# Kernel tuning notes

Measured on AMD Instinct MI355X. Metric: run time of the kernel, lower is better.

## Reference

```python
import jax, jax.numpy as jnp
import numpy as np

B, T, D, H = 2, 2048, 1024, 16
DK = D // H


def setup_inputs() -> dict:
    key = jax.random.key(0)
    ks = jax.random.split(key, 11)
    s = 1.0 / np.sqrt(D)
    return {
        "x_q": jax.random.normal(ks[0], (B, T, D), jnp.float32),
        "x_kv": jax.random.normal(ks[1], (B, T, D), jnp.float32),
        "mask": jnp.ones((B, 1, T, T), jnp.int32),
        "Wq": jax.random.normal(ks[2], (D, D), jnp.float32) * s,
        "bq": jnp.zeros((D,), jnp.float32),
        "Wk": jax.random.normal(ks[3], (D, D), jnp.float32) * s,
        "bk": jnp.zeros((D,), jnp.float32),
        "Wv": jax.random.normal(ks[4], (D, D), jnp.float32) * s,
        "bv": jnp.zeros((D,), jnp.float32),
        "Wo": jax.random.normal(ks[5], (D, D), jnp.float32) * s,
        "bo": jnp.zeros((D,), jnp.float32),
    }


def _split_heads(x):
    # (B, T, D) -> (B, H, T, DK)
    b, t, _ = x.shape
    return x.reshape(b, t, H, DK).transpose(0, 2, 1, 3)


def reference(x_q, x_kv, mask, Wq, bq, Wk, bk, Wv, bv, Wo, bo):
    # Linear layers use torch convention: y = x @ W.T + b
    Q = _split_heads(x_q @ Wq.T + bq)   # (B,H,Tq,DK)
    K = _split_heads(x_kv @ Wk.T + bk)  # (B,H,Tk,DK)
    V = _split_heads(x_kv @ Wv.T + bv)  # (B,H,Tk,DK)

    scores = jnp.einsum("bhqd,bhkd->bhqk", Q, K) / jnp.sqrt(jnp.float32(DK))
    scores = jnp.where(mask == 0, jnp.float32(-jnp.inf), scores)
    attn = jax.nn.softmax(scores, axis=-1)  # (B,H,Tq,Tk)

    out = jnp.einsum("bhqk,bhkd->bhqd", attn, V)
    out = out.transpose(0, 2, 1, 3).reshape(B, T, D)  # combine heads
    out = out @ Wo.T + bo
    return out, attn
```

## Files before the change

kernel.cpp:

```cpp
#include <hip/hip_runtime.h>
#include <hip/hip_bf16.h>

#define DEVINL __device__ __forceinline__

typedef __attribute__((ext_vector_type(4))) float f32x4;
typedef __attribute__((ext_vector_type(8))) short short8;
typedef __attribute__((ext_vector_type(4))) short short4v;

constexpr int CB = 2, CT = 2048, CD = 1024, CH = 16, CDK = 64;
constexpr int CM = CB * CT;
constexpr float LOG2E = 1.44269504088896340736f;

DEVINL ushort f2bf(float f) {
  __hip_bfloat16 h = __float2bfloat16(f);
  ushort u; __builtin_memcpy(&u, &h, 2); return u;
}

DEVINL float bf2f(ushort u) {
  uint x = ((uint)u) << 16; float f; __builtin_memcpy(&f, &x, 4); return f;
}

DEVINL void gl2lds16(const ushort* g, ushort* ldsbase) {
  __builtin_amdgcn_global_load_lds(
      (const __attribute__((address_space(1))) void*)g,
      (__attribute__((address_space(3))) void*)ldsbase, 16, 0, 0);
}

__global__ void prep_kernel(const float* __restrict__ s0, ushort* __restrict__ d0, int n0,
                            const float* __restrict__ s1, ushort* __restrict__ d1, int n1,
                            const float* __restrict__ s2, ushort* __restrict__ d2, int n2,
                            const float* __restrict__ s3, ushort* __restrict__ d3, int n3,
                            const float* __restrict__ s4, ushort* __restrict__ d4, int n4,
                            const float* __restrict__ s5, ushort* __restrict__ d5, int n5,
                            const int* __restrict__ mask, uint* __restrict__ flags,
                            int cvt_blocks)
{
  if ((int)blockIdx.x >= cvt_blocks) {
    const int tile = blockIdx.x - cvt_blocks;
    const int b = tile >> 10, qb = (tile >> 5) & 31, kb = tile & 31;
    const int* base = mask + ((size_t)b * CT + qb * 64) * CT + kb * 64;
    const int r = threadIdx.x >> 2, c0 = (threadIdx.x & 3) * 16;
    int ok = 1;
    for (int j = 0; j < 4; ++j) {
      int4 v = *reinterpret_cast<const int4*>(base + (size_t)r * CT + c0 + j * 4);
      ok &= (v.x != 0) & (v.y != 0) & (v.z != 0) & (v.w != 0);
    }
    __shared__ int red[4];
    unsigned long long bal = __ballot(ok);
    if ((threadIdx.x & 63) == 0) red[threadIdx.x >> 6] = (bal == ~0ull);
    __syncthreads();
    if (threadIdx.x == 0) flags[tile] = (uint)(red[0] & red[1] & red[2] & red[3]);
    return;
  }
  int i = (blockIdx.x * blockDim.x + threadIdx.x) * 4;
  const float* s; ushort* d;
  if (i < n0) { s = s0; d = d0; }
  else if ((i -= n0) < n1) { s = s1; d = d1; }
  else if ((i -= n1) < n2) { s = s2; d = d2; }
  else if ((i -= n2) < n3) { s = s3; d = d3; }
  else if ((i -= n3) < n4) { s = s4; d = d4; }
  else if ((i -= n4) < n5) { s = s5; d = d5; }
  else return;
  float4 v = *reinterpret_cast<const float4*>(s + i);
  ushort4 o;
  o.x = f2bf(v.x); o.y = f2bf(v.y); o.z = f2bf(v.z); o.w = f2bf(v.w);
  *reinterpret_cast<ushort4*>(d + i) = o;
}

__global__ __launch_bounds__(256, 2)
void gemm_nt_kernel(const ushort* __restrict__ A, const ushort* __restrict__ Bm,
                    const float* __restrict__ bias1, const float* __restrict__ bias2,
                    void* __restrict__ Out, void* __restrict__ Out2,
                    int M, int N, int K, int mode, float scale)
{
  constexpr int BM = 128, BN = 64, BK = 32;
  __shared__ __align__(16) ushort As[2][BM * BK];
  __shared__ __align__(16) ushort Bs[2][BN * BK];
  const int tid = threadIdx.x;
  const int lane = tid & 63, wid = tid >> 6;
  const int wr = wid >> 1, wc = wid & 1;
  const int bm0 = blockIdx.y * BM, bn0 = blockIdx.x * BN;
  const int rsel = lane & 15, ksel = (lane >> 4) * 8;
  const int srow = lane >> 2, sc8 = (lane & 3) * 8;

  f32x4 acc[4][2];
  for (int i = 0; i < 4; ++i) for (int j = 0; j < 2; ++j) acc[i][j] = f32x4{0.f, 0.f, 0.f, 0.f};

  auto stage = [&](int bu, int k0) {
    const int ra0 = wid * 32;
    gl2lds16(&A[(size_t)(bm0 + ra0 + srow) * K + k0 + sc8],      &As[bu][ra0 * BK]);
    gl2lds16(&A[(size_t)(bm0 + ra0 + 16 + srow) * K + k0 + sc8], &As[bu][(ra0 + 16) * BK]);
    const int rb0 = wid * 16;
    gl2lds16(&Bm[(size_t)(bn0 + rb0 + srow) * K + k0 + sc8],     &Bs[bu][rb0 * BK]);
  };

  stage(0, 0);
  __syncthreads();
  const int NKT = K / BK;
  int bu = 0;
  for (int kt = 0; kt < NKT; ++kt) {
    if (kt + 1 < NKT) stage(bu ^ 1, (kt + 1) * BK);
    short8 af[4], bfr[2];
    for (int mi = 0; mi < 4; ++mi)
      af[mi] = *reinterpret_cast<short8*>(&As[bu][(wr * 64 + mi * 16 + rsel) * BK + ksel]);
    for (int ni = 0; ni < 2; ++ni)
      bfr[ni] = *reinterpret_cast<short8*>(&Bs[bu][(wc * 32 + ni * 16 + rsel) * BK + ksel]);
    for (int mi = 0; mi < 4; ++mi)
      for (int ni = 0; ni < 2; ++ni)
        acc[mi][ni] = __builtin_amdgcn_mfma_f32_16x16x32_bf16(af[mi], bfr[ni], acc[mi][ni], 0, 0, 0);
    if (kt + 1 < NKT) { __syncthreads(); bu ^= 1; }
  }

  const int r0 = (lane >> 4) * 4;
  for (int mi = 0; mi < 4; ++mi)
    for (int ni = 0; ni < 2; ++ni) {
      int gj = bn0 + wc * 32 + ni * 16 + rsel;
      float bv = (mode == 3 && gj >= 1024) ? bias2[gj - 1024] : bias1[gj];
      for (int r = 0; r < 4; ++r) {
        int gi = bm0 + wr * 64 + mi * 16 + r0 + r;
        float v = (acc[mi][ni][r] + bv) * scale;
        if (mode == 2) {
          reinterpret_cast<float*>(Out)[(size_t)gi * N + gj] = v;
        } else {
          int bb = gi >> 11, t = gi & (CT - 1);
          if (mode == 3 && gj >= 1024) {
            int gjv = gj - 1024;
            reinterpret_cast<ushort*>(Out2)[(((size_t)(bb * CH + (gjv >> 6)) * CDK + (gjv & 63)) * CT + t)] = f2bf(v);
          } else {
            reinterpret_cast<ushort*>(Out)[(((size_t)(bb * CH + (gj >> 6)) * CT + t) * CDK + (gj & 63))] = f2bf(v);
          }
        }
      }
    }
}

__global__ __launch_bounds__(512, 2)
void attn_kernel(const ushort* __restrict__ Qb, const ushort* __restrict__ Kb,
                 const ushort* __restrict__ Vt, const int* __restrict__ mask,
                 const uint* __restrict__ flags,
                 float* __restrict__ attn_out, ushort* __restrict__ oh)
{
  __shared__ __align__(16) ushort Ks[2][64 * 64];
  __shared__ __align__(16) ushort Vs[2][64 * 64];
  __shared__ __align__(16) ushort Pf[8][16 * 64];

  const int tid = threadIdx.x, wid = tid >> 6, lane = tid & 63;
  const int bh = blockIdx.y, b = bh >> 4, h = bh & 15;
  const int q0A = blockIdx.x * 256 + wid * 16;
  const int q0B = q0A + 128;
  const int rsel = lane & 15, grp = lane >> 4, ksel = grp * 8;
  const int swz = rsel & 7;
  const uint* flA = flags + (b << 10) + ((q0A >> 6) << 5);
  const uint* flB = flags + (b << 10) + ((q0B >> 6) << 5);
  const ushort* kpan = Kb + (size_t)bh * CT * CDK;
  const ushort* vpan = Vt + (size_t)bh * CDK * CT;

  const int strow = tid >> 3, stc = (tid & 7) ^ (strow & 7);

  auto stageK = [&](int bu, int k0) {
    gl2lds16(&kpan[(size_t)(k0 + strow) * CDK + stc * 8], &Ks[bu][(size_t)wid * 512]);
  };
  auto stageV = [&](int bu, int k0) {
    gl2lds16(&vpan[(size_t)strow * CT + k0 + stc * 8], &Vs[bu][(size_t)wid * 512]);
  };

  short8 qaA0, qaA1, qaB0, qaB1;
  {
    const ushort* qrowA = Qb + ((size_t)bh * CT + q0A + rsel) * CDK;
    qaA0 = *reinterpret_cast<const short8*>(qrowA + ksel);
    qaA1 = *reinterpret_cast<const short8*>(qrowA + 32 + ksel);
    const ushort* qrowB = Qb + ((size_t)bh * CT + q0B + rsel) * CDK;
    qaB0 = *reinterpret_cast<const short8*>(qrowB + ksel);
    qaB1 = *reinterpret_cast<const short8*>(qrowB + 32 + ksel);
  }

  const int* mrow = mask + (size_t)b * CT * CT;
  const int qmeA = q0A + rsel, qmeB = q0B + rsel;
  float* apan = attn_out + (size_t)bh * CT * CT;
  ushort* pw = &Pf[wid][0];

  float lA = 0.f;
  stageK(0, 0);
  __syncthreads();
  int bu = 0;
  for (int kt = 0; kt < 32; ++kt) {
    const int k0 = kt * 64;
    if (kt + 1 < 32) stageK(bu ^ 1, k0 + 64);
    const uint f = flA[kt];
    for (int ni = 0; ni < 4; ++ni) {
      const int krow = ni * 16 + rsel;
      short8 kb0 = *reinterpret_cast<short8*>(&Ks[bu][krow * 64 + ((grp    ) ^ swz) * 8]);
      short8 kb1 = *reinterpret_cast<short8*>(&Ks[bu][krow * 64 + ((grp + 4) ^ swz) * 8]);
      f32x4 z = {0.f, 0.f, 0.f, 0.f};
      z = __builtin_amdgcn_mfma_f32_16x16x32_bf16(kb0, qaA0, z, 0, 0, 0);
      z = __builtin_amdgcn_mfma_f32_16x16x32_bf16(kb1, qaA1, z, 0, 0, 0);
      if (f) {
        lA += exp2f(z[0]) + exp2f(z[1]) + exp2f(z[2]) + exp2f(z[3]);
      } else {
        const int kb_ = k0 + ni * 16 + grp * 4;
        for (int r = 0; r < 4; ++r)
          lA += mrow[(size_t)qmeA * CT + kb_ + r] ? exp2f(z[r]) : 0.f;
      }
    }
    __syncthreads();
    bu ^= 1;
  }
  lA += __shfl_xor(lA, 16, 64);
  lA += __shfl_xor(lA, 32, 64);
  const float llA = __log2f(lA);

  f32x4 oacc[4];
  for (int nd = 0; nd < 4; ++nd) oacc[nd] = f32x4{0.f, 0.f, 0.f, 0.f};
  float lB = 0.f;

  stageK(0, 0);
  stageV(0, 0);
  asm volatile("s_waitcnt vmcnt(0)" ::: "memory");
  __builtin_amdgcn_s_barrier();
  asm volatile("" ::: "memory");
  bu = 0;
  for (int kt = 0; kt < 32; ++kt) {
    const int k0 = kt * 64;
    if (kt + 1 < 32) { stageK(bu ^ 1, k0 + 64); stageV(bu ^ 1, k0 + 64); }
    asm volatile("" ::: "memory");
    const uint fA = flA[kt], fB = flB[kt];
    for (int ni = 0; ni < 4; ++ni) {
      const int krow = ni * 16 + rsel;
      short8 kb0 = *reinterpret_cast<short8*>(&Ks[bu][krow * 64 + ((grp    ) ^ swz) * 8]);
      short8 kb1 = *reinterpret_cast<short8*>(&Ks[bu][krow * 64 + ((grp + 4) ^ swz) * 8]);
      {
        f32x4 z = {0.f, 0.f, 0.f, 0.f};
        z = __builtin_amdgcn_mfma_f32_16x16x32_bf16(kb0, qaB0, z, 0, 0, 0);
        z = __builtin_amdgcn_mfma_f32_16x16x32_bf16(kb1, qaB1, z, 0, 0, 0);
        if (fB) {
          lB += exp2f(z[0]) + exp2f(z[1]) + exp2f(z[2]) + exp2f(z[3]);
        } else {
          const int kb_ = k0 + ni * 16 + grp * 4;
          for (int r = 0; r < 4; ++r)
            lB += mrow[(size_t)qmeB * CT + kb_ + r] ? exp2f(z[r]) : 0.f;
        }
      }
      f32x4 z = {0.f, 0.f, 0.f, 0.f};
      z = __builtin_amdgcn_mfma_f32_16x16x32_bf16(kb0, qaA0, z, 0, 0, 0);
      z = __builtin_amdgcn_mfma_f32_16x16x32_bf16(kb1, qaA1, z, 0, 0, 0);
      float p0, p1, p2, p3;
      if (fA) {
        p0 = exp2f(z[0] - llA); p1 = exp2f(z[1] - llA);
        p2 = exp2f(z[2] - llA); p3 = exp2f(z[3] - llA);
      } else {
        const size_t mb = (size_t)qmeA * CT + k0 + ni * 16 + grp * 4;
        p0 = mrow[mb + 0] ? exp2f(z[0] - llA) : 0.f;
        p1 = mrow[mb + 1] ? exp2f(z[1] - llA) : 0.f;
        p2 = mrow[mb + 2] ? exp2f(z[2] - llA) : 0.f;
        p3 = mrow[mb + 3] ? exp2f(z[3] - llA) : 0.f;
      }
      const int chpos = (2 * ni + (grp >> 1)) ^ swz;
      short4v pk = {(short)f2bf(p0), (short)f2bf(p1), (short)f2bf(p2), (short)f2bf(p3)};
      *reinterpret_cast<short4v*>(&pw[rsel * 64 + chpos * 8 + (grp & 1) * 4]) = pk;
    }
    for (int rr = 0; rr < 4; ++rr) {
      const int row = rr * 4 + grp;
      const int rs = row & 7;
      short4v pv4 = *reinterpret_cast<short4v*>(
          &pw[row * 64 + (((rsel >> 1) ^ rs)) * 8 + (rsel & 1) * 4]);
      f32x4 v = {bf2f((ushort)pv4[0]), bf2f((ushort)pv4[1]),
                 bf2f((ushort)pv4[2]), bf2f((ushort)pv4[3])};
      __builtin_nontemporal_store(v,
          reinterpret_cast<f32x4*>(apan + (size_t)(q0A + row) * CT + k0 + rsel * 4));
    }
    short8 pa0 = *reinterpret_cast<short8*>(&pw[rsel * 64 + ((grp    ) ^ swz) * 8]);
    short8 pa1 = *reinterpret_cast<short8*>(&pw[rsel * 64 + ((grp + 4) ^ swz) * 8]);
    for (int nd = 0; nd < 4; ++nd) {
      const int vrow = nd * 16 + rsel;
      short8 vb0 = *reinterpret_cast<short8*>(&Vs[bu][vrow * 64 + ((grp    ) ^ swz) * 8]);
      short8 vb1 = *reinterpret_cast<short8*>(&Vs[bu][vrow * 64 + ((grp + 4) ^ swz) * 8]);
      oacc[nd] = __builtin_amdgcn_mfma_f32_16x16x32_bf16(pa0, vb0, oacc[nd], 0, 0, 0);
      oacc[nd] = __builtin_amdgcn_mfma_f32_16x16x32_bf16(pa1, vb1, oacc[nd], 0, 0, 0);
    }
    asm volatile("s_waitcnt vmcnt(4)" ::: "memory");
    __builtin_amdgcn_s_barrier();
    asm volatile("" ::: "memory");
    bu ^= 1;
  }
  for (int nd = 0; nd < 4; ++nd)
    for (int r = 0; r < 4; ++r) {
      int q = q0A + grp * 4 + r, d = nd * 16 + rsel;
      oh[((size_t)b * CT + q) * CD + h * CDK + d] = f2bf(oacc[nd][r]);
    }
  lB += __shfl_xor(lB, 16, 64);
  lB += __shfl_xor(lB, 32, 64);
  const float llB = __log2f(lB);

  for (int nd = 0; nd < 4; ++nd) oacc[nd] = f32x4{0.f, 0.f, 0.f, 0.f};
  stageK(0, 0);
  stageV(0, 0);
  asm volatile("s_waitcnt vmcnt(0)" ::: "memory");
  __builtin_amdgcn_s_barrier();
  asm volatile("" ::: "memory");
  bu = 0;
  for (int kt = 0; kt < 32; ++kt) {
    const int k0 = kt * 64;
    if (kt + 1 < 32) { stageK(bu ^ 1, k0 + 64); stageV(bu ^ 1, k0 + 64); }
    asm volatile("" ::: "memory");
    const uint f = flB[kt];
    for (int ni = 0; ni < 4; ++ni) {
      const int krow = ni * 16 + rsel;
      short8 kb0 = *reinterpret_cast<short8*>(&Ks[bu][krow * 64 + ((grp    ) ^ swz) * 8]);
      short8 kb1 = *reinterpret_cast<short8*>(&Ks[bu][krow * 64 + ((grp + 4) ^ swz) * 8]);
      f32x4 z = {0.f, 0.f, 0.f, 0.f};
      z = __builtin_amdgcn_mfma_f32_16x16x32_bf16(kb0, qaB0, z, 0, 0, 0);
      z = __builtin_amdgcn_mfma_f32_16x16x32_bf16(kb1, qaB1, z, 0, 0, 0);
      float p0, p1, p2, p3;
      if (f) {
        p0 = exp2f(z[0] - llB); p1 = exp2f(z[1] - llB);
        p2 = exp2f(z[2] - llB); p3 = exp2f(z[3] - llB);
      } else {
        const size_t mb = (size_t)qmeB * CT + k0 + ni * 16 + grp * 4;
        p0 = mrow[mb + 0] ? exp2f(z[0] - llB) : 0.f;
        p1 = mrow[mb + 1] ? exp2f(z[1] - llB) : 0.f;
        p2 = mrow[mb + 2] ? exp2f(z[2] - llB) : 0.f;
        p3 = mrow[mb + 3] ? exp2f(z[3] - llB) : 0.f;
      }
      const int chpos = (2 * ni + (grp >> 1)) ^ swz;
      short4v pk = {(short)f2bf(p0), (short)f2bf(p1), (short)f2bf(p2), (short)f2bf(p3)};
      *reinterpret_cast<short4v*>(&pw[rsel * 64 + chpos * 8 + (grp & 1) * 4]) = pk;
    }
    for (int rr = 0; rr < 4; ++rr) {
      const int row = rr * 4 + grp;
      const int rs = row & 7;
      short4v pv4 = *reinterpret_cast<short4v*>(
          &pw[row * 64 + (((rsel >> 1) ^ rs)) * 8 + (rsel & 1) * 4]);
      f32x4 v = {bf2f((ushort)pv4[0]), bf2f((ushort)pv4[1]),
                 bf2f((ushort)pv4[2]), bf2f((ushort)pv4[3])};
      __builtin_nontemporal_store(v,
          reinterpret_cast<f32x4*>(apan + (size_t)(q0B + row) * CT + k0 + rsel * 4));
    }
    short8 pa0 = *reinterpret_cast<short8*>(&pw[rsel * 64 + ((grp    ) ^ swz) * 8]);
    short8 pa1 = *reinterpret_cast<short8*>(&pw[rsel * 64 + ((grp + 4) ^ swz) * 8]);
    for (int nd = 0; nd < 4; ++nd) {
      const int vrow = nd * 16 + rsel;
      short8 vb0 = *reinterpret_cast<short8*>(&Vs[bu][vrow * 64 + ((grp    ) ^ swz) * 8]);
      short8 vb1 = *reinterpret_cast<short8*>(&Vs[bu][vrow * 64 + ((grp + 4) ^ swz) * 8]);
      oacc[nd] = __builtin_amdgcn_mfma_f32_16x16x32_bf16(pa0, vb0, oacc[nd], 0, 0, 0);
      oacc[nd] = __builtin_amdgcn_mfma_f32_16x16x32_bf16(pa1, vb1, oacc[nd], 0, 0, 0);
    }
    asm volatile("s_waitcnt vmcnt(4)" ::: "memory");
    __builtin_amdgcn_s_barrier();
    asm volatile("" ::: "memory");
    bu ^= 1;
  }
  for (int nd = 0; nd < 4; ++nd)
    for (int r = 0; r < 4; ++r) {
      int q = q0B + grp * 4 + r, d = nd * 16 + rsel;
      oh[((size_t)b * CT + q) * CD + h * CDK + d] = f2bf(oacc[nd][r]);
    }
}

extern "C" void kernel_launch(void* const* d_in, const int* in_sizes, int n_in,
                              void* d_out, int out_size, void* d_ws, size_t ws_size,
                              hipStream_t stream)
{
  const float* x_q  = (const float*)d_in[0];
  const float* x_kv = (const float*)d_in[1];
  const int*   mask = (const int*)d_in[2];
  const float* Wq = (const float*)d_in[3];
  const float* bq = (const float*)d_in[4];
  const float* Wk = (const float*)d_in[5];
  const float* bk = (const float*)d_in[6];
  const float* Wv = (const float*)d_in[7];
  const float* bv = (const float*)d_in[8];
  const float* Wo = (const float*)d_in[9];
  const float* bo = (const float*)d_in[10];

  float* out  = (float*)d_out;
  float* attn = out + (size_t)CB * CT * CD;

  char* w = (char*)d_ws;
  auto alloc = [&](size_t bytes) { char* p = w; w += (bytes + 255) & ~(size_t)255; return p; };
  ushort* xq_bf  = (ushort*)alloc((size_t)CM * CD * 2);
  ushort* xkv_bf = (ushort*)alloc((size_t)CM * CD * 2);
  ushort* Wq_bf  = (ushort*)alloc((size_t)CD * CD * 2);
  ushort* Wk_bf  = (ushort*)alloc((size_t)CD * CD * 2);
  ushort* Wv_bf  = (ushort*)alloc((size_t)CD * CD * 2);
  ushort* Wo_bf  = (ushort*)alloc((size_t)CD * CD * 2);
  ushort* Q_bf   = (ushort*)alloc((size_t)CM * CD * 2);
  ushort* K_bf   = (ushort*)alloc((size_t)CM * CD * 2);
  ushort* Vt_bf  = (ushort*)alloc((size_t)CM * CD * 2);
  ushort* oh_bf  = (ushort*)alloc((size_t)CM * CD * 2);
  uint*   mflags = (uint*)alloc(2048 * sizeof(uint));

  {
    const int nx = CM * CD, nw = CD * CD;
    const int cvt_blocks = ((2 * nx + 4 * nw) / 4 + 255) / 256;
    hipLaunchKernelGGL(prep_kernel, dim3(cvt_blocks + 2048), dim3(256), 0, stream,
                       x_q, xq_bf, nx, x_kv, xkv_bf, nx,
                       Wq, Wq_bf, nw, Wk, Wk_bf, nw,
                       Wv, Wv_bf, nw, Wo, Wo_bf, nw,
                       mask, mflags, cvt_blocks);
  }

  hipLaunchKernelGGL(gemm_nt_kernel, dim3(CD / 64, CM / 128), dim3(256), 0, stream,
                     xq_bf, Wq_bf, bq, bq, (void*)Q_bf, nullptr, CM, CD, CD, 0, 0.125f * LOG2E);
  hipLaunchKernelGGL(gemm_nt_kernel, dim3(2 * CD / 64, CM / 128), dim3(256), 0, stream,
                     xkv_bf, Wk_bf, bk, bv, (void*)K_bf, (void*)Vt_bf, CM, 2 * CD, CD, 3, 1.0f);

  hipLaunchKernelGGL(attn_kernel, dim3(CT / 256, CB * CH), dim3(512), 0, stream,
                     Q_bf, K_bf, Vt_bf, mask, mflags, attn, oh_bf);

  hipLaunchKernelGGL(gemm_nt_kernel, dim3(CD / 64, CM / 128), dim3(256), 0, stream,
                     oh_bf, Wo_bf, bo, bo, d_out, nullptr, CM, CD, CD, 2, 1.0f);
}
```

Measured before the change: 281.7 us.

## Triple-buffer K/V tiles in attention output passes with deeper prefetch

The two attention passes that compute the probabilities and P·V now stage K and V tiles through a three-slot LDS ring, prefetching two tiles ahead instead of one. The vmcnt waits are retuned so the stores still in flight can stay outstanding across more iterations. This is meant to hide global-to-LDS load latency behind the MFMA and softmax work. In exchange it uses more LDS per block, which could reduce occupancy at two blocks per CU, and the hand-counted vmcnt values risk waiting too little or too long.

```diff
diff --git a/kernel.cpp b/kernel.cpp
--- a/kernel.cpp
+++ b/kernel.cpp
@@ -140,8 +140,8 @@
                  const uint* __restrict__ flags,
                  float* __restrict__ attn_out, ushort* __restrict__ oh)
 {
-  __shared__ __align__(16) ushort Ks[2][64 * 64];
-  __shared__ __align__(16) ushort Vs[2][64 * 64];
+  __shared__ __align__(16) ushort Ks[3][64 * 64];
+  __shared__ __align__(16) ushort Vs[3][64 * 64];
   __shared__ __align__(16) ushort Pf[8][16 * 64];
 
   const int tid = threadIdx.x, wid = tid >> 6, lane = tid & 63;
@@ -213,21 +213,21 @@
   for (int nd = 0; nd < 4; ++nd) oacc[nd] = f32x4{0.f, 0.f, 0.f, 0.f};
   float lB = 0.f;
 
-  stageK(0, 0);
-  stageV(0, 0);
+  stageK(0, 0);   stageV(0, 0);
+  stageK(1, 64);  stageV(1, 64);
   asm volatile("s_waitcnt vmcnt(0)" ::: "memory");
   __builtin_amdgcn_s_barrier();
   asm volatile("" ::: "memory");
-  bu = 0;
   for (int kt = 0; kt < 32; ++kt) {
     const int k0 = kt * 64;
-    if (kt + 1 < 32) { stageK(bu ^ 1, k0 + 64); stageV(bu ^ 1, k0 + 64); }
+    if (kt + 2 < 32) { stageK((kt + 2) % 3, k0 + 128); stageV((kt + 2) % 3, k0 + 128); }
     asm volatile("" ::: "memory");
+    const int cb = kt % 3;
     const uint fA = flA[kt], fB = flB[kt];
     for (int ni = 0; ni < 4; ++ni) {
       const int krow = ni * 16 + rsel;
-      short8 kb0 = *reinterpret_cast<short8*>(&Ks[bu][krow * 64 + ((grp    ) ^ swz) * 8]);
-      short8 kb1 = *reinterpret_cast<short8*>(&Ks[bu][krow * 64 + ((grp + 4) ^ swz) * 8]);
+      short8 kb0 = *reinterpret_cast<short8*>(&Ks[cb][krow * 64 + ((grp    ) ^ swz) * 8]);
+      short8 kb1 = *reinterpret_cast<short8*>(&Ks[cb][krow * 64 + ((grp + 4) ^ swz) * 8]);
       {
         f32x4 z = {0.f, 0.f, 0.f, 0.f};
         z = __builtin_amdgcn_mfma_f32_16x16x32_bf16(kb0, qaB0, z, 0, 0, 0);
@@ -272,16 +272,16 @@
     short8 pa1 = *reinterpret_cast<short8*>(&pw[rsel * 64 + ((grp + 4) ^ swz) * 8]);
     for (int nd = 0; nd < 4; ++nd) {
       const int vrow = nd * 16 + rsel;
-      short8 vb0 = *reinterpret_cast<short8*>(&Vs[bu][vrow * 64 + ((grp    ) ^ swz) * 8]);
-      short8 vb1 = *reinterpret_cast<short8*>(&Vs[bu][vrow * 64 + ((grp + 4) ^ swz) * 8]);
+      short8 vb0 = *reinterpret_cast<short8*>(&Vs[cb][vrow * 64 + ((grp    ) ^ swz) * 8]);
+      short8 vb1 = *reinterpret_cast<short8*>(&Vs[cb][vrow * 64 + ((grp + 4) ^ swz) * 8]);
       oacc[nd] = __builtin_amdgcn_mfma_f32_16x16x32_bf16(pa0, vb0, oacc[nd], 0, 0, 0);
       oacc[nd] = __builtin_amdgcn_mfma_f32_16x16x32_bf16(pa1, vb1, oacc[nd], 0, 0, 0);
     }
-    asm volatile("s_waitcnt vmcnt(4)" ::: "memory");
-    __builtin_amdgcn_s_barrier();
-    asm volatile("" ::: "memory");
-    bu ^= 1;
-  }
+    if (kt < 30)       asm volatile("s_waitcnt vmcnt(10)" ::: "memory");
+    else if (kt == 30) asm volatile("s_waitcnt vmcnt(8)"  ::: "memory");
+    if (kt < 31) { __builtin_amdgcn_s_barrier(); asm volatile("" ::: "memory"); }
+  }
+  __syncthreads();
   for (int nd = 0; nd < 4; ++nd)
     for (int r = 0; r < 4; ++r) {
       int q = q0A + grp * 4 + r, d = nd * 16 + rsel;
@@ -292,21 +292,21 @@
   const float llB = __log2f(lB);
 
   for (int nd = 0; nd < 4; ++nd) oacc[nd] = f32x4{0.f, 0.f, 0.f, 0.f};
-  stageK(0, 0);
-  stageV(0, 0);
+  stageK(0, 0);   stageV(0, 0);
+  stageK(1, 64);  stageV(1, 64);
   asm volatile("s_waitcnt vmcnt(0)" ::: "memory");
   __builtin_amdgcn_s_barrier();
   asm volatile("" ::: "memory");
-  bu = 0;
   for (int kt = 0; kt < 32; ++kt) {
     const int k0 = kt * 64;
-    if (kt + 1 < 32) { stageK(bu ^ 1, k0 + 64); stageV(bu ^ 1, k0 + 64); }
+    if (kt + 2 < 32) { stageK((kt + 2) % 3, k0 + 128); stageV((kt + 2) % 3, k0 + 128); }
     asm volatile("" ::: "memory");
+    const int cb = kt % 3;
     const uint f = flB[kt];
     for (int ni = 0; ni < 4; ++ni) {
       const int krow = ni * 16 + rsel;
-      short8 kb0 = *reinterpret_cast<short8*>(&Ks[bu][krow * 64 + ((grp    ) ^ swz) * 8]);
-      short8 kb1 = *reinterpret_cast<short8*>(&Ks[bu][krow * 64 + ((grp + 4) ^ swz) * 8]);
+      short8 kb0 = *reinterpret_cast<short8*>(&Ks[cb][krow * 64 + ((grp    ) ^ swz) * 8]);
+      short8 kb1 = *reinterpret_cast<short8*>(&Ks[cb][krow * 64 + ((grp + 4) ^ swz) * 8]);
       f32x4 z = {0.f, 0.f, 0.f, 0.f};
       z = __builtin_amdgcn_mfma_f32_16x16x32_bf16(kb0, qaB0, z, 0, 0, 0);
       z = __builtin_amdgcn_mfma_f32_16x16x32_bf16(kb1, qaB1, z, 0, 0, 0);
@@ -339,15 +339,14 @@
     short8 pa1 = *reinterpret_cast<short8*>(&pw[rsel * 64 + ((grp + 4) ^ swz) * 8]);
     for (int nd = 0; nd < 4; ++nd) {
       const int vrow = nd * 16 + rsel;
-      short8 vb0 = *reinterpret_cast<short8*>(&Vs[bu][vrow * 64 + ((grp    ) ^ swz) * 8]);
-      short8 vb1 = *reinterpret_cast<short8*>(&Vs[bu][vrow * 64 + ((grp + 4) ^ swz) * 8]);
+      short8 vb0 = *reinterpret_cast<short8*>(&Vs[cb][vrow * 64 + ((grp    ) ^ swz) * 8]);
+      short8 vb1 = *reinterpret_cast<short8*>(&Vs[cb][vrow * 64 + ((grp + 4) ^ swz) * 8]);
       oacc[nd] = __builtin_amdgcn_mfma_f32_16x16x32_bf16(pa0, vb0, oacc[nd], 0, 0, 0);
       oacc[nd] = __builtin_amdgcn_mfma_f32_16x16x32_bf16(pa1, vb1, oacc[nd], 0, 0, 0);
     }
-    asm volatile("s_waitcnt vmcnt(4)" ::: "memory");
-    __builtin_amdgcn_s_barrier();
-    asm volatile("" ::: "memory");
-    bu ^= 1;
+    if (kt < 30)       asm volatile("s_waitcnt vmcnt(10)" ::: "memory");
+    else if (kt == 30) asm volatile("s_waitcnt vmcnt(8)"  ::: "memory");
+    if (kt < 31) { __builtin_amdgcn_s_barrier(); asm volatile("" ::: "memory"); }
   }
   for (int nd = 0; nd < 4; ++nd)
     for (int r = 0; r < 4; ++r) {
```

After: 286.6 us. About the same (+1.7%).
